# Kernel tuning notes

Hardware: AMD Instinct MI355X
Metric: run time of the kernel (lower is better)

The kernel has to match this reference:

```python
import jax, jax.numpy as jnp
import numpy as np

NUM_CLASSES = 81
THRESHOLD = 0.5
NEGPOS_RATIO = 3
VAR0, VAR1 = 0.1, 0.2
B, P, T = 64, 25000, 16


def setup_inputs() -> dict:
    key = jax.random.key(0)
    k1, k2, k3, k4, k5, k6 = jax.random.split(key, 6)
    loc_data = jax.random.normal(k1, (B, P, 4), dtype=jnp.float32)
    conf_data = jax.random.normal(k2, (B, P, NUM_CLASSES), dtype=jnp.float32)
    # priors in center-offset form (cx, cy, w, h), all in (0,1), w/h > 0
    centers = jax.random.uniform(k3, (P, 2), minval=0.05, maxval=0.95)
    wh = jax.random.uniform(k4, (P, 2), minval=0.05, maxval=0.3)
    priors = jnp.concatenate([centers, wh], axis=1).astype(jnp.float32)
    # ground-truth boxes in corner form (xmin, ymin, xmax, ymax), valid (max > min)
    pts = jax.random.uniform(k5, (B, T, 2, 2), minval=0.0, maxval=0.98)
    mn = jnp.min(pts, axis=2)
    mx = jnp.max(pts, axis=2) + 0.02  # strictly positive width/height
    boxes = jnp.concatenate([mn, jnp.clip(mx, 0.0, 1.0)], axis=-1)
    labels = jax.random.randint(k6, (B, T), 0, NUM_CLASSES - 1).astype(jnp.float32)
    targets = jnp.concatenate([boxes, labels[..., None]], axis=-1)
    return {"loc_data": loc_data, "conf_data": conf_data, "priors": priors, "targets": targets}


def point_form(p):
    # (cx,cy,w,h) -> (xmin,ymin,xmax,ymax)
    return jnp.concatenate([p[:, :2] - p[:, 2:] / 2, p[:, :2] + p[:, 2:] / 2], axis=1)


def jaccard(a, b):
    # a: [T,4], b: [P,4], corner form -> IoU [T,P]
    lt = jnp.maximum(a[:, None, :2], b[None, :, :2])
    rb = jnp.minimum(a[:, None, 2:], b[None, :, 2:])
    wh = jnp.clip(rb - lt, 0.0)
    inter = wh[..., 0] * wh[..., 1]
    area_a = ((a[:, 2] - a[:, 0]) * (a[:, 3] - a[:, 1]))[:, None]
    area_b = ((b[:, 2] - b[:, 0]) * (b[:, 3] - b[:, 1]))[None, :]
    return inter / (area_a + area_b - inter)


def encode(matched, priors):
    # SSD offset encoding with variances
    g_cxcy = ((matched[:, :2] + matched[:, 2:]) * 0.5 - priors[:, :2]) / (VAR0 * priors[:, 2:])
    g_wh = jnp.log((matched[:, 2:] - matched[:, :2]) / priors[:, 2:]) / VAR1
    return jnp.concatenate([g_cxcy, g_wh], axis=1)


def match_one(truths, labels, priors):
    # truths: [T,4] corner, labels: [T], priors: [P,4] center
    overlaps = jaccard(truths, point_form(priors))        # [T,P]
    best_prior_idx = jnp.argmax(overlaps, axis=1)         # [T]
    best_truth_overlap = jnp.max(overlaps, axis=0)        # [P]
    best_truth_idx = jnp.argmax(overlaps, axis=0)         # [P]
    best_truth_overlap = best_truth_overlap.at[best_prior_idx].set(2.0)
    for j in range(T):
        best_truth_idx = best_truth_idx.at[best_prior_idx[j]].set(j)
    matched = truths[best_truth_idx]                      # [P,4]
    conf = labels[best_truth_idx].astype(jnp.int32) + 1
    conf = jnp.where(best_truth_overlap < THRESHOLD, 0, conf)
    return encode(matched, priors), conf


def smooth_l1(d):
    ad = jnp.abs(d)
    return jnp.where(ad < 1.0, 0.5 * d * d, ad - 0.5)


def reference(loc_data, conf_data, priors, targets):
    truths = jax.lax.stop_gradient(targets[..., :4])  # .data in torch
    labels = jax.lax.stop_gradient(targets[..., 4])
    loc_t, conf_t = jax.vmap(match_one, in_axes=(0, 0, None))(truths, labels, priors)
    pos = conf_t > 0                                      # [B,P]
    num_priors = pos.shape[1]
    # localization: smooth-L1 summed over positive priors (masked instead of boolean gather)
    loss_l = jnp.sum(jnp.where(pos[..., None], smooth_l1(loc_data - loc_t), 0.0))
    # per-prior conf loss = logsumexp - logit[target]
    lse = jax.nn.logsumexp(conf_data, axis=-1)            # [B,P]
    conf_gt = jnp.take_along_axis(conf_data, conf_t[..., None], axis=-1)[..., 0]
    ce = lse - conf_gt
    # hard negative mining: zero positives, double argsort rank
    loss_c = jnp.where(pos, 0.0, ce)
    loss_idx = jnp.argsort(-loss_c, axis=1)
    idx_rank = jnp.argsort(loss_idx, axis=1)
    num_pos = jnp.sum(pos, axis=1, keepdims=True)
    num_neg = jnp.minimum(NEGPOS_RATIO * num_pos, num_priors - 1)
    neg = idx_rank < num_neg
    # cross-entropy summed over positives + mined negatives
    loss_conf = jnp.sum(jnp.where(pos | neg, ce, 0.0))
    N = jnp.maximum(jnp.sum(num_pos).astype(loc_data.dtype), 1.0)
    return loss_l / N, loss_conf / N
```

## Files before the change

### kernel.cpp

```cpp
#include <hip/hip_runtime.h>

namespace {

constexpr int kB = 64;
constexpr int kP = 25000;
constexpr int kT = 16;
constexpr int kC = 81;
constexpr int kRowsPerBlk = 64;
constexpr int kChunks = 16;
constexpr int kChunkP = (kP + kChunks - 1) / kChunks;
constexpr float kThresh = 0.5f;

__device__ __forceinline__ float smooth_l1(float d) {
  float ad = fabsf(d);
  return ad < 1.0f ? 0.5f * d * d : ad - 0.5f;
}

__global__ __launch_bounds__(256) void match1_kernel(
    const float* __restrict__ priors,
    const float* __restrict__ targets,
    unsigned char* __restrict__ mcode,
    unsigned long long* __restrict__ best_prior) {
  const int chunk = blockIdx.x;
  const int b = blockIdx.y;
  const int tid = threadIdx.x;
  const int p0 = chunk * kChunkP;
  const int p1 = min(p0 + kChunkP, kP);

  __shared__ float tx0[kT], ty0[kT], tx1[kT], ty1[kT], tarea[kT];
  __shared__ float smax[kT][256];
  __shared__ int sidx[kT][256];

  if (tid < kT) {
    const float* tg = targets + (b * kT + tid) * 5;
    float x0 = tg[0], y0 = tg[1], x1 = tg[2], y1 = tg[3];
    tx0[tid] = x0; ty0[tid] = y0; tx1[tid] = x1; ty1[tid] = y1;
    tarea[tid] = (x1 - x0) * (y1 - y0);
  }
  __syncthreads();

  float bestv[kT];
  int besti[kT];
#pragma unroll
  for (int t = 0; t < kT; ++t) { bestv[t] = -1.0f; besti[t] = 0; }

  for (int p = p0 + tid; p < p1; p += 256) {
    float4 pr = reinterpret_cast<const float4*>(priors)[p];
    float px0 = pr.x - pr.z * 0.5f, py0 = pr.y - pr.w * 0.5f;
    float px1 = pr.x + pr.z * 0.5f, py1 = pr.y + pr.w * 0.5f;
    float parea = (px1 - px0) * (py1 - py0);
    float mv = -1.0f;
    int mt = 0;
#pragma unroll
    for (int t = 0; t < kT; ++t) {
      float lx = fmaxf(tx0[t], px0), ly = fmaxf(ty0[t], py0);
      float rx = fminf(tx1[t], px1), ry = fminf(ty1[t], py1);
      float w = fmaxf(rx - lx, 0.0f), h = fmaxf(ry - ly, 0.0f);
      float inter = w * h;
      float iou = inter / (tarea[t] + parea - inter);
      if (iou > bestv[t]) { bestv[t] = iou; besti[t] = p; }
      if (iou > mv) { mv = iou; mt = t; }
    }
    mcode[b * kP + p] = (unsigned char)(mt | (mv < kThresh ? 0x80 : 0));
  }
#pragma unroll
  for (int t = 0; t < kT; ++t) { smax[t][tid] = bestv[t]; sidx[t][tid] = besti[t]; }
  __syncthreads();
  for (int s = 128; s > 0; s >>= 1) {
    if (tid < s) {
#pragma unroll
      for (int t = 0; t < kT; ++t) {
        float v1 = smax[t][tid], v2 = smax[t][tid + s];
        int i1 = sidx[t][tid], i2 = sidx[t][tid + s];
        if (v2 > v1 || (v2 == v1 && i2 < i1)) { smax[t][tid] = v2; sidx[t][tid] = i2; }
      }
    }
    __syncthreads();
  }
  if (tid < kT) {
    unsigned long long pk = ((unsigned long long)__float_as_uint(smax[tid][0]) << 32) |
                            (unsigned long long)(0xFFFFFFFFu - (unsigned)sidx[tid][0]);
    atomicMax(&best_prior[b * kT + tid], pk);
  }
}

__global__ __launch_bounds__(256) void match2_kernel(
    const float* __restrict__ loc_data,
    const float* __restrict__ priors,
    const float* __restrict__ targets,
    const unsigned long long* __restrict__ best_prior,
    unsigned char* __restrict__ code,
    int* __restrict__ num_pos,
    float* __restrict__ loss_l_acc) {
  const int chunk = blockIdx.x;
  const int b = blockIdx.y;
  const int tid = threadIdx.x;
  const int p0 = chunk * kChunkP;
  const int p1 = min(p0 + kChunkP, kP);

  __shared__ int s_bp[kT];
  __shared__ float sx0[kT], sy0[kT], sx1[kT], sy1[kT], slab[kT];
  __shared__ float swf[4];
  __shared__ int swi[4];

  if (tid < kT) {
    s_bp[tid] = (int)(0xFFFFFFFFu -
                      (unsigned)(best_prior[b * kT + tid] & 0xFFFFFFFFull));
    const float* tg = targets + (b * kT + tid) * 5;
    sx0[tid] = tg[0]; sy0[tid] = tg[1]; sx1[tid] = tg[2]; sy1[tid] = tg[3];
    slab[tid] = tg[4];
  }
  __syncthreads();

  float lsum = 0.0f;
  int pcount = 0;
  for (int p = p0 + tid; p < p1; p += 256) {
    int c = code[b * kP + p];
    int mt = c & 0x0F;
    bool neg = (c & 0x80) != 0;
    bool forced = false;
#pragma unroll
    for (int j = 0; j < kT; ++j) {
      if (s_bp[j] == p) { mt = j; forced = true; }
    }
    int conf = (!forced && neg) ? 0 : ((int)slab[mt] + 1);
    code[b * kP + p] = (unsigned char)conf;
    if (conf > 0) {
      ++pcount;
      float4 pr = reinterpret_cast<const float4*>(priors)[p];
      float mx0 = sx0[mt], my0 = sy0[mt], mx1 = sx1[mt], my1 = sy1[mt];
      float gcx = ((mx0 + mx1) * 0.5f - pr.x) / (0.1f * pr.z);
      float gcy = ((my0 + my1) * 0.5f - pr.y) / (0.1f * pr.w);
      float gw = logf((mx1 - mx0) / pr.z) / 0.2f;
      float gh = logf((my1 - my0) / pr.w) / 0.2f;
      float4 ld = reinterpret_cast<const float4*>(loc_data)[b * kP + p];
      lsum += smooth_l1(ld.x - gcx) + smooth_l1(ld.y - gcy) +
              smooth_l1(ld.z - gw) + smooth_l1(ld.w - gh);
    }
  }
  for (int off = 32; off > 0; off >>= 1) {
    lsum += __shfl_down(lsum, off, 64);
    pcount += __shfl_down(pcount, off, 64);
  }
  if ((tid & 63) == 0) { swf[tid >> 6] = lsum; swi[tid >> 6] = pcount; }
  __syncthreads();
  if (tid == 0) {
    float lt = swf[0] + swf[1] + swf[2] + swf[3];
    int pt = swi[0] + swi[1] + swi[2] + swi[3];
    if (lt != 0.0f) atomicAdd(loss_l_acc, lt);
    if (pt != 0) atomicAdd(&num_pos[b], pt);
  }
}

__global__ __launch_bounds__(256) void ce_kernel(
    const float* __restrict__ conf_data,
    const unsigned char* __restrict__ conf_t,
    float* __restrict__ loss_c,
    float* __restrict__ pos_ce_acc) {
  __shared__ float tile[kRowsPerBlk * kC];
  __shared__ float swsum[4];
  const int tid = threadIdx.x;
  const long long base = (long long)blockIdx.x * (kRowsPerBlk * kC);
  const float4* src = reinterpret_cast<const float4*>(conf_data + base);
  float4* dst = reinterpret_cast<float4*>(tile);
#pragma unroll
  for (int i = 0; i < 6; ++i) {
    int idx = tid + i * 256;
    if (idx < kRowsPerBlk * kC / 4) dst[idx] = src[idx];
  }
  __syncthreads();

  const int r = tid >> 2;
  const int sub = tid & 3;
  const float* x = tile + r * kC;
  float m = -3.0e38f;
  for (int j = sub; j < kC; j += 4) m = fmaxf(m, x[j]);
  m = fmaxf(m, __shfl_xor(m, 1, 64));
  m = fmaxf(m, __shfl_xor(m, 2, 64));
  float s = 0.0f;
  for (int j = sub; j < kC; j += 4) s += __expf(x[j] - m);
  s += __shfl_xor(s, 1, 64);
  s += __shfl_xor(s, 2, 64);
  float posce = 0.0f;
  if (sub == 0) {
    const long long row = (long long)blockIdx.x * kRowsPerBlk + r;
    float lse = __logf(s) + m;
    int ct = conf_t[row];
    float ce = lse - x[ct];
    bool pos = ct > 0;
    loss_c[row] = pos ? 0.0f : ce;
    posce = pos ? ce : 0.0f;
  }
  for (int off = 32; off > 0; off >>= 1) posce += __shfl_down(posce, off, 64);
  if ((tid & 63) == 0) swsum[tid >> 6] = posce;
  __syncthreads();
  if (tid == 0) {
    float t = swsum[0] + swsum[1] + swsum[2] + swsum[3];
    if (t != 0.0f) atomicAdd(pos_ce_acc, t);
  }
}

__global__ __launch_bounds__(256) void select_kernel(
    const float* __restrict__ loss_c,
    const int* __restrict__ num_pos,
    float* __restrict__ neg_ce_acc) {
  const int b = blockIdx.x;
  const int tid = threadIdx.x;
  const int k = min(3 * num_pos[b], kP - 1);
  __shared__ int swi[4];
  __shared__ float swf[4];
  if (k <= 0) return;

  constexpr int kV4 = kP / 4;
  constexpr int kPer = (kV4 + 255) / 256;
  const float4* v4 = reinterpret_cast<const float4*>(loss_c + (long long)b * kP);
  float4 lv[kPer];
#pragma unroll
  for (int j = 0; j < kPer; ++j) {
    int i = tid + j * 256;
    lv[j] = (i < kV4) ? v4[i] : float4{0.0f, 0.0f, 0.0f, 0.0f};
  }

  unsigned int ans = 0;
  for (int bit = 30; bit >= 0; --bit) {
    const unsigned int cand = ans | (1u << bit);
    int cnt = 0;
#pragma unroll
    for (int j = 0; j < kPer; ++j) {
      cnt += (__float_as_uint(lv[j].x) >= cand) + (__float_as_uint(lv[j].y) >= cand) +
             (__float_as_uint(lv[j].z) >= cand) + (__float_as_uint(lv[j].w) >= cand);
    }
    for (int off = 32; off > 0; off >>= 1) cnt += __shfl_down(cnt, off, 64);
    if ((tid & 63) == 0) swi[tid >> 6] = cnt;
    __syncthreads();
    int tot = swi[0] + swi[1] + swi[2] + swi[3];
    if (tot >= k) ans = cand;
    __syncthreads();
  }
  float sum = 0.0f;
  int cgt = 0;
#pragma unroll
  for (int j = 0; j < kPer; ++j) {
    if (__float_as_uint(lv[j].x) > ans) { sum += lv[j].x; ++cgt; }
    if (__float_as_uint(lv[j].y) > ans) { sum += lv[j].y; ++cgt; }
    if (__float_as_uint(lv[j].z) > ans) { sum += lv[j].z; ++cgt; }
    if (__float_as_uint(lv[j].w) > ans) { sum += lv[j].w; ++cgt; }
  }
  for (int off = 32; off > 0; off >>= 1) {
    sum += __shfl_down(sum, off, 64);
    cgt += __shfl_down(cgt, off, 64);
  }
  if ((tid & 63) == 0) { swf[tid >> 6] = sum; swi[tid >> 6] = cgt; }
  __syncthreads();
  if (tid == 0) {
    float st = swf[0] + swf[1] + swf[2] + swf[3];
    int ct = swi[0] + swi[1] + swi[2] + swi[3];
    atomicAdd(neg_ce_acc, st + (float)(k - ct) * __uint_as_float(ans));
  }
}

__global__ void finalize_kernel(const int* __restrict__ num_pos,
                                const float* __restrict__ acc,
                                float* __restrict__ out) {
  int tid = threadIdx.x;
  int np = num_pos[tid];
  for (int off = 32; off > 0; off >>= 1) np += __shfl_down(np, off, 64);
  if (tid == 0) {
    float N = fmaxf((float)np, 1.0f);
    out[0] = acc[0] / N;
    out[1] = (acc[1] + acc[2]) / N;
  }
}

}

extern "C" void kernel_launch(void* const* d_in, const int* in_sizes, int n_in,
                              void* d_out, int out_size, void* d_ws, size_t ws_size,
                              hipStream_t stream) {
  const float* loc_data = (const float*)d_in[0];
  const float* conf_data = (const float*)d_in[1];
  const float* priors = (const float*)d_in[2];
  const float* targets = (const float*)d_in[3];
  float* out = (float*)d_out;

  char* ws = (char*)d_ws;
  float* loss_c = (float*)ws;
  unsigned char* code = (unsigned char*)(ws + 6400000);
  unsigned long long* best_prior = (unsigned long long*)(ws + 8000000);
  int* num_pos = (int*)(ws + 8008192);
  float* acc = (float*)(ws + 8008448);

  hipMemsetAsync(ws + 8000000, 0, 8512, stream);
  hipLaunchKernelGGL(match1_kernel, dim3(kChunks, kB), dim3(256), 0, stream,
                     priors, targets, code, best_prior);
  hipLaunchKernelGGL(match2_kernel, dim3(kChunks, kB), dim3(256), 0, stream,
                     loc_data, priors, targets, best_prior, code, num_pos, acc + 0);
  hipLaunchKernelGGL(ce_kernel, dim3(kB * kP / kRowsPerBlk), dim3(256), 0, stream,
                     conf_data, code, loss_c, acc + 1);
  hipLaunchKernelGGL(select_kernel, dim3(kB), dim3(256), 0, stream,
                     loss_c, num_pos, acc + 2);
  hipLaunchKernelGGL(finalize_kernel, dim3(1), dim3(64), 0, stream,
                     num_pos, acc, out);
}
```

Measured before the change: 839.3 us.

## Fuse matching kernels via cooperative grid sync and widen select blocks

Merges the two matching passes into one cooperative kernel. Per-prior match codes stay in shared memory across a grid-wide sync instead of being written out and reread, and a kernel launch goes away. The select kernel now uses 1024 threads per block so each thread holds fewer registers of loss values. The cooperative launch needs all 1024 blocks resident at once, and the code falls back to the old two-kernel path if that launch fails.

```diff
diff --git a/kernel.cpp b/kernel.cpp
--- a/kernel.cpp
+++ b/kernel.cpp
@@ -1,4 +1,7 @@
 #include <hip/hip_runtime.h>
+#include <hip/hip_cooperative_groups.h>
+
+namespace cg = cooperative_groups;
 
 namespace {
 
@@ -14,6 +17,136 @@
 __device__ __forceinline__ float smooth_l1(float d) {
   float ad = fabsf(d);
   return ad < 1.0f ? 0.5f * d * d : ad - 0.5f;
+}
+
+__global__ __launch_bounds__(256, 4) void match_fused_kernel(
+    const float* __restrict__ loc_data,
+    const float* __restrict__ priors,
+    const float* __restrict__ targets,
+    unsigned long long* __restrict__ best_prior,
+    unsigned char* __restrict__ code,
+    int* __restrict__ num_pos,
+    float* __restrict__ loss_l_acc) {
+  const int chunk = blockIdx.x;
+  const int b = blockIdx.y;
+  const int tid = threadIdx.x;
+  const int p0 = chunk * kChunkP;
+  const int p1 = min(p0 + kChunkP, kP);
+
+  __shared__ float tx0[kT], ty0[kT], tx1[kT], ty1[kT], tarea[kT], slab[kT];
+  __shared__ unsigned char smcode[kChunkP];
+  __shared__ float swv[kT][4];
+  __shared__ int swi2[kT][4];
+  __shared__ int s_bp[kT];
+  __shared__ float swf[4];
+  __shared__ int swi[4];
+
+  if (tid < kT) {
+    const float* tg = targets + (b * kT + tid) * 5;
+    float x0 = tg[0], y0 = tg[1], x1 = tg[2], y1 = tg[3];
+    tx0[tid] = x0; ty0[tid] = y0; tx1[tid] = x1; ty1[tid] = y1;
+    tarea[tid] = (x1 - x0) * (y1 - y0);
+    slab[tid] = tg[4];
+  }
+  __syncthreads();
+
+  float bestv[kT];
+  int besti[kT];
+#pragma unroll
+  for (int t = 0; t < kT; ++t) { bestv[t] = -1.0f; besti[t] = 0; }
+
+  for (int p = p0 + tid; p < p1; p += 256) {
+    float4 pr = reinterpret_cast<const float4*>(priors)[p];
+    float px0 = pr.x - pr.z * 0.5f, py0 = pr.y - pr.w * 0.5f;
+    float px1 = pr.x + pr.z * 0.5f, py1 = pr.y + pr.w * 0.5f;
+    float parea = (px1 - px0) * (py1 - py0);
+    float mv = -1.0f;
+    int mt = 0;
+#pragma unroll
+    for (int t = 0; t < kT; ++t) {
+      float lx = fmaxf(tx0[t], px0), ly = fmaxf(ty0[t], py0);
+      float rx = fminf(tx1[t], px1), ry = fminf(ty1[t], py1);
+      float w = fmaxf(rx - lx, 0.0f), h = fmaxf(ry - ly, 0.0f);
+      float inter = w * h;
+      float iou = inter / (tarea[t] + parea - inter);
+      if (iou > bestv[t]) { bestv[t] = iou; besti[t] = p; }
+      if (iou > mv) { mv = iou; mt = t; }
+    }
+    smcode[p - p0] = (unsigned char)(mt | (mv < kThresh ? 0x80 : 0));
+  }
+
+#pragma unroll
+  for (int t = 0; t < kT; ++t) {
+    float v = bestv[t];
+    int i = besti[t];
+    for (int off = 32; off > 0; off >>= 1) {
+      float v2 = __shfl_xor(v, off, 64);
+      int i2 = __shfl_xor(i, off, 64);
+      if (v2 > v || (v2 == v && i2 < i)) { v = v2; i = i2; }
+    }
+    if ((tid & 63) == 0) { swv[t][tid >> 6] = v; swi2[t][tid >> 6] = i; }
+  }
+  __syncthreads();
+  if (tid < kT) {
+    float v = swv[tid][0];
+    int i = swi2[tid][0];
+#pragma unroll
+    for (int w = 1; w < 4; ++w) {
+      float v2 = swv[tid][w];
+      int i2 = swi2[tid][w];
+      if (v2 > v || (v2 == v && i2 < i)) { v = v2; i = i2; }
+    }
+    unsigned long long pk = ((unsigned long long)__float_as_uint(v) << 32) |
+                            (unsigned long long)(0xFFFFFFFFu - (unsigned)i);
+    atomicMax(&best_prior[b * kT + tid], pk);
+  }
+
+  cg::this_grid().sync();
+
+  if (tid < kT) {
+    unsigned long long pk = atomicMax(&best_prior[b * kT + tid], 0ull);
+    s_bp[tid] = (int)(0xFFFFFFFFu - (unsigned)(pk & 0xFFFFFFFFull));
+  }
+  __syncthreads();
+
+  float lsum = 0.0f;
+  int pcount = 0;
+  for (int p = p0 + tid; p < p1; p += 256) {
+    int c = smcode[p - p0];
+    int mt = c & 0x0F;
+    bool neg = (c & 0x80) != 0;
+    bool forced = false;
+#pragma unroll
+    for (int j = 0; j < kT; ++j) {
+      if (s_bp[j] == p) { mt = j; forced = true; }
+    }
+    int conf = (!forced && neg) ? 0 : ((int)slab[mt] + 1);
+    code[b * kP + p] = (unsigned char)conf;
+    if (conf > 0) {
+      ++pcount;
+      float4 pr = reinterpret_cast<const float4*>(priors)[p];
+      float mx0 = tx0[mt], my0 = ty0[mt], mx1 = tx1[mt], my1 = ty1[mt];
+      float gcx = ((mx0 + mx1) * 0.5f - pr.x) / (0.1f * pr.z);
+      float gcy = ((my0 + my1) * 0.5f - pr.y) / (0.1f * pr.w);
+      float gw = logf((mx1 - mx0) / pr.z) / 0.2f;
+      float gh = logf((my1 - my0) / pr.w) / 0.2f;
+      float4 ld = reinterpret_cast<const float4*>(loc_data)[b * kP + p];
+      lsum += smooth_l1(ld.x - gcx) + smooth_l1(ld.y - gcy) +
+              smooth_l1(ld.z - gw) + smooth_l1(ld.w - gh);
+    }
+  }
+  for (int off = 32; off > 0; off >>= 1) {
+    lsum += __shfl_down(lsum, off, 64);
+    pcount += __shfl_down(pcount, off, 64);
+  }
+  if ((tid & 63) == 0) { swf[tid >> 6] = lsum; swi[tid >> 6] = pcount; }
+  __syncthreads();
+  if (tid == 0) {
+    float lt = swf[0] + swf[1] + swf[2] + swf[3];
+    int pt = swi[0] + swi[1] + swi[2] + swi[3];
+    if (lt != 0.0f) atomicAdd(loss_l_acc, lt);
+    if (pt != 0) atomicAdd(&num_pos[b], pt);
+  }
 }
 
 __global__ __launch_bounds__(256) void match1_kernel(
@@ -200,24 +333,24 @@
   }
 }
 
-__global__ __launch_bounds__(256) void select_kernel(
+__global__ __launch_bounds__(1024) void select_kernel(
     const float* __restrict__ loss_c,
     const int* __restrict__ num_pos,
     float* __restrict__ neg_ce_acc) {
   const int b = blockIdx.x;
   const int tid = threadIdx.x;
   const int k = min(3 * num_pos[b], kP - 1);
-  __shared__ int swi[4];
-  __shared__ float swf[4];
+  __shared__ int swi[16];
+  __shared__ float swf[16];
   if (k <= 0) return;
 
   constexpr int kV4 = kP / 4;
-  constexpr int kPer = (kV4 + 255) / 256;
+  constexpr int kPer = (kV4 + 1023) / 1024;
   const float4* v4 = reinterpret_cast<const float4*>(loss_c + (long long)b * kP);
   float4 lv[kPer];
 #pragma unroll
   for (int j = 0; j < kPer; ++j) {
-    int i = tid + j * 256;
+    int i = tid + j * 1024;
     lv[j] = (i < kV4) ? v4[i] : float4{0.0f, 0.0f, 0.0f, 0.0f};
   }
 
@@ -233,7 +366,9 @@
     for (int off = 32; off > 0; off >>= 1) cnt += __shfl_down(cnt, off, 64);
     if ((tid & 63) == 0) swi[tid >> 6] = cnt;
     __syncthreads();
-    int tot = swi[0] + swi[1] + swi[2] + swi[3];
+    int tot = 0;
+#pragma unroll
+    for (int w = 0; w < 16; ++w) tot += swi[w];
     if (tot >= k) ans = cand;
     __syncthreads();
   }
@@ -253,8 +388,10 @@
   if ((tid & 63) == 0) { swf[tid >> 6] = sum; swi[tid >> 6] = cgt; }
   __syncthreads();
   if (tid == 0) {
-    float st = swf[0] + swf[1] + swf[2] + swf[3];
-    int ct = swi[0] + swi[1] + swi[2] + swi[3];
+    float st = 0.0f;
+    int ct = 0;
+#pragma unroll
+    for (int w = 0; w < 16; ++w) { st += swf[w]; ct += swi[w]; }
     atomicAdd(neg_ce_acc, st + (float)(k - ct) * __uint_as_float(ans));
   }
 }
@@ -289,15 +426,25 @@
   unsigned long long* best_prior = (unsigned long long*)(ws + 8000000);
   int* num_pos = (int*)(ws + 8008192);
   float* acc = (float*)(ws + 8008448);
+  float* loss_l_acc = acc;
 
   hipMemsetAsync(ws + 8000000, 0, 8512, stream);
-  hipLaunchKernelGGL(match1_kernel, dim3(kChunks, kB), dim3(256), 0, stream,
-                     priors, targets, code, best_prior);
-  hipLaunchKernelGGL(match2_kernel, dim3(kChunks, kB), dim3(256), 0, stream,
-                     loc_data, priors, targets, best_prior, code, num_pos, acc + 0);
+
+  void* margs[] = {(void*)&loc_data, (void*)&priors,    (void*)&targets,
+                   (void*)&best_prior, (void*)&code,    (void*)&num_pos,
+                   (void*)&loss_l_acc};
+  hipError_t cerr = hipLaunchCooperativeKernel(
+      (const void*)match_fused_kernel, dim3(kChunks, kB), dim3(256), margs, 0,
+      stream);
+  if (cerr != hipSuccess) {
+    hipLaunchKernelGGL(match1_kernel, dim3(kChunks, kB), dim3(256), 0, stream,
+                       priors, targets, code, best_prior);
+    hipLaunchKernelGGL(match2_kernel, dim3(kChunks, kB), dim3(256), 0, stream,
+                       loc_data, priors, targets, best_prior, code, num_pos, acc + 0);
+  }
   hipLaunchKernelGGL(ce_kernel, dim3(kB * kP / kRowsPerBlk), dim3(256), 0, stream,
                      conf_data, code, loss_c, acc + 1);
-  hipLaunchKernelGGL(select_kernel, dim3(kB), dim3(256), 0, stream,
+  hipLaunchKernelGGL(select_kernel, dim3(kB), dim3(1024), 0, stream,
                      loss_c, num_pos, acc + 2);
   hipLaunchKernelGGL(finalize_kernel, dim3(1), dim3(64), 0, stream,
                      num_pos, acc, out);
```

New measurement: 946.5 us. 12.8% more time.
